# Kernel tuning notes

Hardware: AMD Instinct MI355X
Metric: run time of the kernel (lower is better)

The kernel has to match this reference:

```python
import jax, jax.numpy as jnp
import numpy as np

ROI_SIZE = 14  # hard-coded in the torch module


def _bilinear(feature, x, y):
    """feature: [B,C,H,W]; x, y: arbitrary (matching) shape S of sample coords.
    Returns [B, C, *S]. Matches torch code: corner indices are clamped BEFORE
    the interpolation weights are computed from them."""
    H, W = feature.shape[-2:]
    y1 = jnp.clip(jnp.floor(y).astype(jnp.int32), 0, H - 1)
    y2 = jnp.clip(jnp.floor(y).astype(jnp.int32) + 1, 0, H - 1)
    x1 = jnp.clip(jnp.floor(x).astype(jnp.int32), 0, W - 1)
    x2 = jnp.clip(jnp.floor(x).astype(jnp.int32) + 1, 0, W - 1)
    wx_lo = x - x1  # weight toward x2 column
    wx_hi = x2 - x  # weight toward x1 column
    wy_lo = y - y1
    wy_hi = y2 - y
    p = feature[:, :, y1, x1] * wx_hi + feature[:, :, y1, x2] * wx_lo
    q = feature[:, :, y2, x1] * wx_hi + feature[:, :, y2, x2] * wx_lo
    return p * wy_hi + q * wy_lo


def setup_inputs() -> dict:
    key = jax.random.key(0)
    kf, k1, k2, k3, k4 = jax.random.split(key, 5)
    B, C, H, W, R = 1, 256, 200, 320, 128
    feature = jax.random.normal(kf, (B, C, H, W), dtype=jnp.float32)
    y1 = jax.random.uniform(k1, (R,), minval=0.0, maxval=H * 0.5)
    x1 = jax.random.uniform(k2, (R,), minval=0.0, maxval=W * 0.5)
    hh = jax.random.uniform(k3, (R,), minval=8.0, maxval=H * 0.45)
    ww = jax.random.uniform(k4, (R,), minval=8.0, maxval=W * 0.45)
    rois = jnp.stack([y1, x1, y1 + hh, x1 + ww], axis=-1).astype(jnp.float32)
    return {"feature": feature, "rois": rois}


def reference(feature, rois):
    R = rois.shape[0]
    B, C, H, W = feature.shape
    sh = (rois[:, 2] - rois[:, 0]) / ROI_SIZE  # [R] bin height stride
    sw = (rois[:, 3] - rois[:, 1]) / ROI_SIZE  # [R] bin width stride
    m = jnp.arange(ROI_SIZE, dtype=rois.dtype)
    y_base = rois[:, 0:1] + sh[:, None] * m  # [R, M]
    x_base = rois[:, 1:2] + sw[:, None] * m  # [R, N]
    frac = jnp.array([1.0 / 3.0, 2.0 / 3.0], dtype=rois.dtype)
    ys = y_base[:, :, None] + sh[:, None, None] * frac  # [R, M, 2]
    xs = x_base[:, :, None] + sw[:, None, None] * frac  # [R, N, 2]
    # all 4 (y, x) sample-point combos per bin -> [R, M, N, 2, 2]
    yy = jnp.broadcast_to(ys[:, :, None, :, None], (R, ROI_SIZE, ROI_SIZE, 2, 2))
    xx = jnp.broadcast_to(xs[:, None, :, None, :], (R, ROI_SIZE, ROI_SIZE, 2, 2))
    samples = _bilinear(feature, xx, yy)  # [B, C, R, M, N, 2, 2]
    # Faithful to torch.max(tensor) with NO dim: global max over B, C, R and
    # the 4 sample points, giving one scalar per bin (m, n).
    bin_max = jnp.max(samples, axis=(0, 1, 2, 5, 6))  # [M, N]
    return jnp.broadcast_to(bin_max, (R, C, ROI_SIZE, ROI_SIZE))
```

## Files before the change

kernel.cpp:

```cpp
#include <hip/hip_runtime.h>
#include <float.h>

#define CC 256
#define HH 200
#define WW 320
#define HW (HH * WW)
#define MM 14
#define SPAN_MAX 144
#define SPAN_PAD 145
#define NCH 8
#define CG 4
#define CPB (CC / CG)

__global__ void roi_init(float* __restrict__ binmax) {
    int t = blockIdx.x * blockDim.x + threadIdx.x;
    if (t < MM * MM) binmax[t] = -FLT_MAX;
}

__device__ inline void atomicMaxF(float* addr, float val) {
    if (val >= 0.0f) {
        atomicMax((int*)addr, __float_as_int(val));
    } else {
        atomicMin((unsigned int*)addr, __float_as_uint(val));
    }
}

__global__ __launch_bounds__(256, 8) void roi_reduce(
    const float* __restrict__ feature,
    const float* __restrict__ rois,
    float* __restrict__ binmax)
{
    const int bid = blockIdx.x;
    const int cg  = bid & (CG - 1);
    const int rm  = bid >> 2;
    const int m   = rm % MM;
    const int r   = rm / MM;
    const int tid = threadIdx.x;
    const int cbase = cg * CPB;

    const float ry1 = rois[r * 4 + 0];
    const float rx1 = rois[r * 4 + 1];
    const float ry2 = rois[r * 4 + 2];
    const float rx2 = rois[r * 4 + 3];
    const float sh = (ry2 - ry1) * (1.0f / 14.0f);
    const float sw = (rx2 - rx1) * (1.0f / 14.0f);
    const float f13 = 1.0f / 3.0f, f23 = 2.0f / 3.0f;

    const float yA = ry1 + sh * (float)m + sh * f13;
    const float yB = ry1 + sh * (float)m + sh * f23;
    const int y1A = min(max((int)floorf(yA), 0), HH - 1);
    const int y2A = min(max((int)floorf(yA) + 1, 0), HH - 1);
    const int y1B = min(max((int)floorf(yB), 0), HH - 1);
    const int y2B = min(max((int)floorf(yB) + 1, 0), HH - 1);
    const float wyloA = yA - (float)y1A, wyhiA = (float)y2A - yA;
    const float wyloB = yB - (float)y1B, wyhiB = (float)y2B - yB;

    const float xmin = rx1 + sw * f13;
    const float xmax = rx1 + sw * 13.0f + sw * f23;
    int xlo = min(max((int)floorf(xmin), 0), WW - 1);
    int xhi = min(max((int)floorf(xmax) + 1, 0), WW - 1);
    int span = xhi - xlo + 1;
    if (span > SPAN_MAX) span = SPAN_MAX;

    const int s  = tid % 56;
    const int cs = tid / 56;
    const int n  = s >> 2;
    const int j  = (s >> 1) & 1;
    const int i  = s & 1;
    const bool active = (tid < 224);

    float wxlo = 0.f, wxhi = 0.f, wylo = 0.f, wyhi = 0.f;
    int c0 = 0, c1 = 0, ra = 0, rb = 1;
    if (active) {
        float x = rx1 + sw * (float)n + sw * (j ? f23 : f13);
        int x1c = min(max((int)floorf(x), 0), WW - 1);
        int x2c = min(max((int)floorf(x) + 1, 0), WW - 1);
        wxlo = x - (float)x1c;
        wxhi = (float)x2c - x;
        c0 = min(max(x1c - xlo, 0), span - 1);
        c1 = min(max(x2c - xlo, 0), span - 1);
        if (i == 0) { ra = 0; rb = 1; wylo = wyloA; wyhi = wyhiA; }
        else        { ra = 2; rb = 3; wylo = wyloB; wyhi = wyhiB; }
    }

    __shared__ float tile[NCH][4][SPAN_PAD];
    __shared__ float pmax[224];

    const int rg   = tid >> 6;
    const int lane = tid & 63;
    const int myrow = (rg == 0) ? y1A : (rg == 1) ? y2A : (rg == 2) ? y1B : y2B;
    const int rowoff = myrow * WW + xlo;

    float lmax = -FLT_MAX;

    for (int cc = 0; cc < CPB; cc += NCH) {
        const float* src = feature + (cbase + cc) * HW + rowoff;
        __syncthreads();
        for (int col = lane; col < span; col += 64) {
            float tmp[NCH];
            #pragma unroll
            for (int ch = 0; ch < NCH; ++ch) tmp[ch] = src[ch * HW + col];
            #pragma unroll
            for (int ch = 0; ch < NCH; ++ch) tile[ch][rg][col] = tmp[ch];
        }
        __syncthreads();
        if (active) {
            #pragma unroll
            for (int q = 0; q < 2; ++q) {
                const int ch = cs * 2 + q;
                float v11 = tile[ch][ra][c0];
                float v12 = tile[ch][ra][c1];
                float v21 = tile[ch][rb][c0];
                float v22 = tile[ch][rb][c1];
                float p = v11 * wxhi + v12 * wxlo;
                float q2 = v21 * wxhi + v22 * wxlo;
                lmax = fmaxf(lmax, p * wyhi + q2 * wylo);
            }
        }
    }

    if (active) pmax[tid] = lmax;
    __syncthreads();
    if (tid < MM) {
        float v = -FLT_MAX;
        #pragma unroll
        for (int c4 = 0; c4 < 4; ++c4)
            #pragma unroll
            for (int q4 = 0; q4 < 4; ++q4)
                v = fmaxf(v, pmax[c4 * 56 + tid * 4 + q4]);
        atomicMaxF(&binmax[m * MM + tid], v);
    }
}

__global__ __launch_bounds__(256) void roi_bcast(
    const float* __restrict__ binmax, float4* __restrict__ out, int total4)
{
    __shared__ float4 b4[49];
    int t = threadIdx.x;
    if (t < 49) b4[t] = ((const float4*)binmax)[t];
    __syncthreads();
    int idx = blockIdx.x * 256 + t;
    if (idx < total4) out[idx] = b4[idx % 49];
}

extern "C" void kernel_launch(void* const* d_in, const int* in_sizes, int n_in,
                              void* d_out, int out_size, void* d_ws, size_t ws_size,
                              hipStream_t stream) {
    const float* feature = (const float*)d_in[0];
    const float* rois    = (const float*)d_in[1];
    float* binmax = (float*)d_ws;
    float* out    = (float*)d_out;

    const int R = in_sizes[1] / 4;

    roi_init<<<1, 256, 0, stream>>>(binmax);
    roi_reduce<<<R * MM * CG, 256, 0, stream>>>(feature, rois, binmax);

    const int total4 = out_size / 4;
    roi_bcast<<<(total4 + 255) / 256, 256, 0, stream>>>(binmax, (float4*)out, total4);
}
```

Baseline: 146.0 us.

## Double-buffer ROI tile loads with direct global-to-LDS async copies

```diff
diff --git a/kernel.cpp b/kernel.cpp
--- a/kernel.cpp
+++ b/kernel.cpp
@@ -1,16 +1,18 @@
 #include <hip/hip_runtime.h>
 #include <float.h>
+#include <stdint.h>
 
 #define CC 256
 #define HH 200
 #define WW 320
 #define HW (HH * WW)
 #define MM 14
-#define SPAN_MAX 144
-#define SPAN_PAD 145
 #define NCH 8
 #define CG 4
 #define CPB (CC / CG)
+#define NR (CPB / NCH)
+#define SP4 38
+#define SPF (SP4 * 4)
 
 __global__ void roi_init(float* __restrict__ binmax) {
     int t = blockIdx.x * blockDim.x + threadIdx.x;
@@ -25,7 +27,14 @@
     }
 }
 
-__global__ __launch_bounds__(256, 8) void roi_reduce(
+__device__ __forceinline__ void gload_lds16(const float* g, float* l) {
+    __builtin_amdgcn_global_load_lds(
+        (const __attribute__((address_space(1))) unsigned int*)g,
+        (__attribute__((address_space(3))) unsigned int*)l,
+        16, 0, 0);
+}
+
+__global__ __launch_bounds__(256, 4) void roi_reduce(
     const float* __restrict__ feature,
     const float* __restrict__ rois,
     float* __restrict__ binmax)
@@ -59,8 +68,10 @@
     const float xmax = rx1 + sw * 13.0f + sw * f23;
     int xlo = min(max((int)floorf(xmin), 0), WW - 1);
     int xhi = min(max((int)floorf(xmax) + 1, 0), WW - 1);
-    int span = xhi - xlo + 1;
-    if (span > SPAN_MAX) span = SPAN_MAX;
+    const int xlo4 = xlo & ~3;
+    int span = xhi - xlo4 + 1;
+    if (span > 4 * SP4 - 4) span = 4 * SP4 - 4;
+    const int span4 = (span + 3) >> 2;
 
     const int s  = tid % 56;
     const int cs = tid / 56;
@@ -77,46 +88,66 @@
         int x2c = min(max((int)floorf(x) + 1, 0), WW - 1);
         wxlo = x - (float)x1c;
         wxhi = (float)x2c - x;
-        c0 = min(max(x1c - xlo, 0), span - 1);
-        c1 = min(max(x2c - xlo, 0), span - 1);
+        c0 = min(max(x1c - xlo4, 0), span - 1);
+        c1 = min(max(x2c - xlo4, 0), span - 1);
         if (i == 0) { ra = 0; rb = 1; wylo = wyloA; wyhi = wyhiA; }
         else        { ra = 2; rb = 3; wylo = wyloB; wyhi = wyhiB; }
     }
 
-    __shared__ float tile[NCH][4][SPAN_PAD];
+    __shared__ float tileF[2][NCH][4][SPF];
     __shared__ float pmax[224];
 
     const int rg   = tid >> 6;
     const int lane = tid & 63;
     const int myrow = (rg == 0) ? y1A : (rg == 1) ? y2A : (rg == 2) ? y1B : y2B;
-    const int rowoff = myrow * WW + xlo;
+    const float* gRow = feature + cbase * HW + myrow * WW + xlo4 + (lane << 2);
+    const bool ld = lane < span4;
+
+    if (ld) {
+        const float* g = gRow;
+        #pragma unroll
+        for (int ch = 0; ch < NCH; ++ch) {
+            gload_lds16(g, &tileF[0][ch][rg][0]);
+            g += HW;
+        }
+    }
 
     float lmax = -FLT_MAX;
+    for (int r8 = 0; r8 < NR; ++r8) {
+        const int b = r8 & 1;
+        if (r8 + 1 < NR) {
+            if (ld) {
+                const float* g = gRow + (r8 + 1) * NCH * HW;
+                #pragma unroll
+                for (int ch = 0; ch < NCH; ++ch) {
+                    gload_lds16(g, &tileF[b ^ 1][ch][rg][0]);
+                    g += HW;
+                }
+            }
+            asm volatile("s_waitcnt vmcnt(8)" ::: "memory");
+        } else {
+            asm volatile("s_waitcnt vmcnt(0)" ::: "memory");
+        }
+        __builtin_amdgcn_s_barrier();
+        asm volatile("" ::: "memory");
 
-    for (int cc = 0; cc < CPB; cc += NCH) {
-        const float* src = feature + (cbase + cc) * HW + rowoff;
-        __syncthreads();
-        for (int col = lane; col < span; col += 64) {
-            float tmp[NCH];
-            #pragma unroll
-            for (int ch = 0; ch < NCH; ++ch) tmp[ch] = src[ch * HW + col];
-            #pragma unroll
-            for (int ch = 0; ch < NCH; ++ch) tile[ch][rg][col] = tmp[ch];
-        }
-        __syncthreads();
         if (active) {
             #pragma unroll
             for (int q = 0; q < 2; ++q) {
-                const int ch = cs * 2 + q;
-                float v11 = tile[ch][ra][c0];
-                float v12 = tile[ch][ra][c1];
-                float v21 = tile[ch][rb][c0];
-                float v22 = tile[ch][rb][c1];
-                float p = v11 * wxhi + v12 * wxlo;
+                const int ch = (cs << 1) | q;
+                const float* ta = &tileF[b][ch][ra][0];
+                const float* tb = &tileF[b][ch][rb][0];
+                float v11 = ta[c0], v12 = ta[c1];
+                float v21 = tb[c0], v22 = tb[c1];
+                float p  = v11 * wxhi + v12 * wxlo;
                 float q2 = v21 * wxhi + v22 * wxlo;
                 lmax = fmaxf(lmax, p * wyhi + q2 * wylo);
             }
         }
+
+        asm volatile("s_waitcnt lgkmcnt(0)" ::: "memory");
+        __builtin_amdgcn_s_barrier();
+        asm volatile("" ::: "memory");
     }
 
     if (active) pmax[tid] = lmax;
@@ -139,8 +170,9 @@
     int t = threadIdx.x;
     if (t < 49) b4[t] = ((const float4*)binmax)[t];
     __syncthreads();
-    int idx = blockIdx.x * 256 + t;
-    if (idx < total4) out[idx] = b4[idx % 49];
+    const int stride = gridDim.x * 256;
+    for (int idx = blockIdx.x * 256 + t; idx < total4; idx += stride)
+        out[idx] = b4[idx % 49];
 }
 
 extern "C" void kernel_launch(void* const* d_in, const int* in_sizes, int n_in,
@@ -157,5 +189,7 @@
     roi_reduce<<<R * MM * CG, 256, 0, stream>>>(feature, rois, binmax);
 
     const int total4 = out_size / 4;
-    roi_bcast<<<(total4 + 255) / 256, 256, 0, stream>>>(binmax, (float4*)out, total4);
+    int nb = (total4 + 255) / 256;
+    if (nb > 2048) nb = 2048;
+    roi_bcast<<<nb, 256, 0, stream>>>(binmax, (float4*)out, total4);
 }
```

Result: slower. 162.7 us (+11.4%).

## Register-prefetch next channel chunk during compute and grid-stride broadcast kernel

Applied to the files above, without the earlier changes.

```diff
diff --git a/kernel.cpp b/kernel.cpp
--- a/kernel.cpp
+++ b/kernel.cpp
@@ -11,6 +11,7 @@
 #define NCH 8
 #define CG 4
 #define CPB (CC / CG)
+#define NR (CPB / NCH)
 
 __global__ void roi_init(float* __restrict__ binmax) {
     int t = blockIdx.x * blockDim.x + threadIdx.x;
@@ -89,21 +90,54 @@
     const int rg   = tid >> 6;
     const int lane = tid & 63;
     const int myrow = (rg == 0) ? y1A : (rg == 1) ? y2A : (rg == 2) ? y1B : y2B;
-    const int rowoff = myrow * WW + xlo;
+    const float* src0 = feature + cbase * HW + myrow * WW + xlo;
 
+    const int colA = lane;
+    const int colB = lane + 64;
+    const int colC = lane + 128;
+    const bool mA = colA < span;
+    const bool mB = colB < span;
+    const bool mC = colC < span;
+
+    float tA[NCH], tB[NCH], tC[NCH];
+
+    #define ISSUE(cc) do {                                                   \
+        const float* s_ = src0 + (cc) * HW;                                  \
+        if (mA) { _Pragma("unroll")                                          \
+            for (int ch = 0; ch < NCH; ++ch) tA[ch] = s_[ch * HW + colA]; }  \
+        if (mB) { _Pragma("unroll")                                          \
+            for (int ch = 0; ch < NCH; ++ch) tB[ch] = s_[ch * HW + colB]; }  \
+        if (mC) { _Pragma("unroll")                                          \
+            for (int ch = 0; ch < NCH; ++ch) tC[ch] = s_[ch * HW + colC]; }  \
+    } while (0)
+
+    ISSUE(0);
     float lmax = -FLT_MAX;
 
-    for (int cc = 0; cc < CPB; cc += NCH) {
-        const float* src = feature + (cbase + cc) * HW + rowoff;
-        __syncthreads();
-        for (int col = lane; col < span; col += 64) {
-            float tmp[NCH];
+    for (int k = 0; k < NR; ++k) {
+        asm volatile("s_waitcnt vmcnt(0)" ::: "memory");
+        __builtin_amdgcn_s_barrier();
+        asm volatile("" ::: "memory");
+
+        if (mA) {
             #pragma unroll
-            for (int ch = 0; ch < NCH; ++ch) tmp[ch] = src[ch * HW + col];
+            for (int ch = 0; ch < NCH; ++ch) tile[ch][rg][colA] = tA[ch];
+        }
+        if (mB) {
             #pragma unroll
-            for (int ch = 0; ch < NCH; ++ch) tile[ch][rg][col] = tmp[ch];
+            for (int ch = 0; ch < NCH; ++ch) tile[ch][rg][colB] = tB[ch];
         }
-        __syncthreads();
+        if (mC) {
+            #pragma unroll
+            for (int ch = 0; ch < NCH; ++ch) tile[ch][rg][colC] = tC[ch];
+        }
+
+        if (k + 1 < NR) ISSUE((k + 1) * NCH);
+
+        asm volatile("s_waitcnt lgkmcnt(0)" ::: "memory");
+        __builtin_amdgcn_s_barrier();
+        asm volatile("" ::: "memory");
+
         if (active) {
             #pragma unroll
             for (int q = 0; q < 2; ++q) {
@@ -112,12 +146,13 @@
                 float v12 = tile[ch][ra][c1];
                 float v21 = tile[ch][rb][c0];
                 float v22 = tile[ch][rb][c1];
-                float p = v11 * wxhi + v12 * wxlo;
+                float p  = v11 * wxhi + v12 * wxlo;
                 float q2 = v21 * wxhi + v22 * wxlo;
                 lmax = fmaxf(lmax, p * wyhi + q2 * wylo);
             }
         }
     }
+    #undef ISSUE
 
     if (active) pmax[tid] = lmax;
     __syncthreads();
@@ -139,8 +174,9 @@
     int t = threadIdx.x;
     if (t < 49) b4[t] = ((const float4*)binmax)[t];
     __syncthreads();
-    int idx = blockIdx.x * 256 + t;
-    if (idx < total4) out[idx] = b4[idx % 49];
+    const int stride = gridDim.x * 256;
+    for (int idx = blockIdx.x * 256 + t; idx < total4; idx += stride)
+        out[idx] = b4[idx % 49];
 }
 
 extern "C" void kernel_launch(void* const* d_in, const int* in_sizes, int n_in,
@@ -157,5 +193,7 @@
     roi_reduce<<<R * MM * CG, 256, 0, stream>>>(feature, rois, binmax);
 
     const int total4 = out_size / 4;
-    roi_bcast<<<(total4 + 255) / 256, 256, 0, stream>>>(binmax, (float4*)out, total4);
+    int nb = (total4 + 255) / 256;
+    if (nb > 2048) nb = 2048;
+    roi_bcast<<<nb, 256, 0, stream>>>(binmax, (float4*)out, total4);
 }
```

After: 146.9 us. Within noise of the previous version (+0.6%).

## Replace LDS row staging with direct per-thread float2 gathers; grid-stride broadcast

Applied to the files above, without the earlier changes.

```diff
diff --git a/kernel.cpp b/kernel.cpp
--- a/kernel.cpp
+++ b/kernel.cpp
@@ -6,11 +6,9 @@
 #define WW 320
 #define HW (HH * WW)
 #define MM 14
-#define SPAN_MAX 144
-#define SPAN_PAD 145
-#define NCH 8
 #define CG 4
 #define CPB (CC / CG)
+#define KPW 16
 
 __global__ void roi_init(float* __restrict__ binmax) {
     int t = blockIdx.x * blockDim.x + threadIdx.x;
@@ -36,7 +34,10 @@
     const int m   = rm % MM;
     const int r   = rm / MM;
     const int tid = threadIdx.x;
-    const int cbase = cg * CPB;
+    const int w    = tid >> 6;
+    const int lane = tid & 63;
+    const int s    = (lane < 56) ? lane : 55;
+    const int cbase = cg * CPB + w * KPW;
 
     const float ry1 = rois[r * 4 + 0];
     const float rx1 = rois[r * 4 + 1];
@@ -46,80 +47,44 @@
     const float sw = (rx2 - rx1) * (1.0f / 14.0f);
     const float f13 = 1.0f / 3.0f, f23 = 2.0f / 3.0f;
 
-    const float yA = ry1 + sh * (float)m + sh * f13;
-    const float yB = ry1 + sh * (float)m + sh * f23;
-    const int y1A = min(max((int)floorf(yA), 0), HH - 1);
-    const int y2A = min(max((int)floorf(yA) + 1, 0), HH - 1);
-    const int y1B = min(max((int)floorf(yB), 0), HH - 1);
-    const int y2B = min(max((int)floorf(yB) + 1, 0), HH - 1);
-    const float wyloA = yA - (float)y1A, wyhiA = (float)y2A - yA;
-    const float wyloB = yB - (float)y1B, wyhiB = (float)y2B - yB;
+    const int nn = s >> 2;
+    const int jj = (s >> 1) & 1;
+    const int ii = s & 1;
 
-    const float xmin = rx1 + sw * f13;
-    const float xmax = rx1 + sw * 13.0f + sw * f23;
-    int xlo = min(max((int)floorf(xmin), 0), WW - 1);
-    int xhi = min(max((int)floorf(xmax) + 1, 0), WW - 1);
-    int span = xhi - xlo + 1;
-    if (span > SPAN_MAX) span = SPAN_MAX;
+    const float y = ry1 + sh * (float)m + sh * (ii ? f23 : f13);
+    const float x = rx1 + sw * (float)nn + sw * (jj ? f23 : f13);
 
-    const int s  = tid % 56;
-    const int cs = tid / 56;
-    const int n  = s >> 2;
-    const int j  = (s >> 1) & 1;
-    const int i  = s & 1;
-    const bool active = (tid < 224);
+    const int y1c = min(max((int)floorf(y), 0), HH - 1);
+    const int y2c = min(max((int)floorf(y) + 1, 0), HH - 1);
+    const int x1c = min(max((int)floorf(x), 0), WW - 1);
+    const int x2c = min(max((int)floorf(x) + 1, 0), WW - 1);
+    const float wylo = y - (float)y1c, wyhi = (float)y2c - y;
+    const float wxlo = x - (float)x1c, wxhi = (float)x2c - x;
+    const bool csel = (x2c == x1c);
 
-    float wxlo = 0.f, wxhi = 0.f, wylo = 0.f, wyhi = 0.f;
-    int c0 = 0, c1 = 0, ra = 0, rb = 1;
-    if (active) {
-        float x = rx1 + sw * (float)n + sw * (j ? f23 : f13);
-        int x1c = min(max((int)floorf(x), 0), WW - 1);
-        int x2c = min(max((int)floorf(x) + 1, 0), WW - 1);
-        wxlo = x - (float)x1c;
-        wxhi = (float)x2c - x;
-        c0 = min(max(x1c - xlo, 0), span - 1);
-        c1 = min(max(x2c - xlo, 0), span - 1);
-        if (i == 0) { ra = 0; rb = 1; wylo = wyloA; wyhi = wyhiA; }
-        else        { ra = 2; rb = 3; wylo = wyloB; wyhi = wyhiB; }
-    }
+    typedef float f2v __attribute__((ext_vector_type(2)));
+    typedef f2v __attribute__((aligned(4))) f2u;
 
-    __shared__ float tile[NCH][4][SPAN_PAD];
-    __shared__ float pmax[224];
-
-    const int rg   = tid >> 6;
-    const int lane = tid & 63;
-    const int myrow = (rg == 0) ? y1A : (rg == 1) ? y2A : (rg == 2) ? y1B : y2B;
-    const int rowoff = myrow * WW + xlo;
+    const float* pA = feature + (size_t)cbase * HW + y1c * WW + x1c;
+    const float* pB = feature + (size_t)cbase * HW + y2c * WW + x1c;
 
     float lmax = -FLT_MAX;
 
-    for (int cc = 0; cc < CPB; cc += NCH) {
-        const float* src = feature + (cbase + cc) * HW + rowoff;
-        __syncthreads();
-        for (int col = lane; col < span; col += 64) {
-            float tmp[NCH];
-            #pragma unroll
-            for (int ch = 0; ch < NCH; ++ch) tmp[ch] = src[ch * HW + col];
-            #pragma unroll
-            for (int ch = 0; ch < NCH; ++ch) tile[ch][rg][col] = tmp[ch];
-        }
-        __syncthreads();
-        if (active) {
-            #pragma unroll
-            for (int q = 0; q < 2; ++q) {
-                const int ch = cs * 2 + q;
-                float v11 = tile[ch][ra][c0];
-                float v12 = tile[ch][ra][c1];
-                float v21 = tile[ch][rb][c0];
-                float v22 = tile[ch][rb][c1];
-                float p = v11 * wxhi + v12 * wxlo;
-                float q2 = v21 * wxhi + v22 * wxlo;
-                lmax = fmaxf(lmax, p * wyhi + q2 * wylo);
-            }
-        }
+    #pragma unroll 4
+    for (int kk = 0; kk < KPW; ++kk) {
+        f2v a = *(const f2u*)pA;
+        f2v b = *(const f2u*)pB;
+        pA += HW;
+        pB += HW;
+        float ax2 = csel ? a.x : a.y;
+        float bx2 = csel ? b.x : b.y;
+        float p = a.x * wxhi + ax2 * wxlo;
+        float q = b.x * wxhi + bx2 * wxlo;
+        lmax = fmaxf(lmax, p * wyhi + q * wylo);
     }
 
-    if (active) pmax[tid] = lmax;
+    __shared__ float pmax[224];
+    if (lane < 56) pmax[w * 56 + s] = lmax;
     __syncthreads();
     if (tid < MM) {
         float v = -FLT_MAX;
@@ -139,8 +104,9 @@
     int t = threadIdx.x;
     if (t < 49) b4[t] = ((const float4*)binmax)[t];
     __syncthreads();
-    int idx = blockIdx.x * 256 + t;
-    if (idx < total4) out[idx] = b4[idx % 49];
+    const int stride = gridDim.x * 256;
+    for (int idx = blockIdx.x * 256 + t; idx < total4; idx += stride)
+        out[idx] = b4[idx % 49];
 }
 
 extern "C" void kernel_launch(void* const* d_in, const int* in_sizes, int n_in,
@@ -157,5 +123,7 @@
     roi_reduce<<<R * MM * CG, 256, 0, stream>>>(feature, rois, binmax);
 
     const int total4 = out_size / 4;
-    roi_bcast<<<(total4 + 255) / 256, 256, 0, stream>>>(binmax, (float4*)out, total4);
+    int nb = (total4 + 255) / 256;
+    if (nb > 2048) nb = 2048;
+    roi_bcast<<<nb, 256, 0, stream>>>(binmax, (float4*)out, total4);
 }
```

Result: no change. 143.9 us (-1.4%).
